# Optimization experiments

Measured on AMD Instinct MI355X. Metric: run time of the kernel, lower is better.

## Reference

```python
import jax, jax.numpy as jnp
import numpy as np

TOPK = 64  # init kwarg: number of dst routes kept per src node


def setup_inputs() -> dict:
    key = jax.random.key(0)
    ks = jax.random.split(key, 6)
    B, J, K, D, Dd = 4, 4096, 8192, 64, 64  # batch, src_nodes, dst_nodes, src_dim, dst_dim
    val = jax.random.normal(ks[0], (B, J, D), jnp.float32)
    state = jax.random.normal(ks[1], (B, J), jnp.float32)
    dst_state = jax.random.normal(ks[2], (B, K), jnp.float32)
    dst_val = jax.random.normal(ks[3], (B, K, Dd), jnp.float32)
    W_route = jax.random.normal(ks[4], (D, K), jnp.float32) / np.sqrt(D).astype(np.float32)
    W_val = jax.random.normal(ks[5], (D, Dd), jnp.float32) / np.sqrt(D).astype(np.float32)
    return dict(val=val, state=state, dst_state=dst_state, dst_val=dst_val,
                W_route=W_route, W_val=W_val)


def _sparse_routes(logits, topk):
    # top-k indices per src node, scatter a bool mask, masked softmax over dst axis
    _, idx = jax.lax.top_k(logits, topk)              # [B, J, topk]
    B, J, K = logits.shape
    mask = jnp.zeros((B, J, K), dtype=bool)
    mask = mask.at[jnp.arange(B)[:, None, None],
                   jnp.arange(J)[None, :, None], idx].set(True)
    neg = jnp.finfo(logits.dtype).min
    return jax.nn.softmax(jnp.where(mask, logits, neg), axis=-1)


def reference(val, state, dst_state, dst_val, W_route, W_val):
    # route_fn: linear over src val -> logits [B, J, K]
    logits = jnp.einsum('bjd,dk->bjk', val, W_route)
    routes = _sparse_routes(logits, TOPK)             # sparse masked softmax
    projected_val = jnp.einsum('bjd,de->bje', val, W_val)  # val_proj_fn (Linear)
    projected_state = state                            # state_proj_fn = Identity
    sender = jax.nn.softplus(state)                    # state_activation_fn
    weighted = routes * sender[..., None]              # [B, J, K]
    delta_state = jnp.einsum('bjk,bj->bk', weighted, projected_state)
    delta_val = jnp.einsum('bjk,bjd->bkd', weighted, projected_val)
    # merge_mode='add'
    return (dst_state + delta_state, dst_val + delta_val)
```

## Files before the change

kernel.cpp:

```cpp
#include <hip/hip_runtime.h>
#include <math.h>

#define NB 4
#define J 4096
#define KDIM 8192
#define DDIM 64
#define DD 64
#define TOPK 64

#define BM 32
#define THREADS 512
#define NITER 16
#define CAP 256
#define BCAP 96
#define OVFCAP (NB * J * TOPK)

typedef _Float16 half8_t __attribute__((ext_vector_type(8)));
typedef float f32x16 __attribute__((ext_vector_type(16)));
union H8 { half8_t h; uint4 u; };
__device__ __forceinline__ half8_t as_h8(uint4 v) { H8 x; x.u = v; return x.h; }

__device__ __forceinline__ unsigned f2key(float f) {
  unsigned u = __float_as_uint(f);
  return u ^ (unsigned)(((int)u >> 31) | 0x80000000);
}
__device__ __forceinline__ float key2f(unsigned k) {
  unsigned u = (k & 0x80000000u) ? (k & 0x7FFFFFFFu) : ~k;
  return __uint_as_float(u);
}
__device__ __forceinline__ unsigned wred_maxu(unsigned v) {
  #pragma unroll
  for (int o = 32; o > 0; o >>= 1) { unsigned u = __shfl_xor(v, o, 64); v = u > v ? u : v; }
  return v;
}
__device__ __forceinline__ unsigned wred_minu(unsigned v) {
  #pragma unroll
  for (int o = 32; o > 0; o >>= 1) { unsigned u = __shfl_xor(v, o, 64); v = u < v ? u : v; }
  return v;
}
__device__ __forceinline__ float wred_addf(float v) {
  #pragma unroll
  for (int o = 32; o > 0; o >>= 1) v += __shfl_xor(v, o, 64);
  return v;
}

__device__ __forceinline__ void route_append(
    unsigned* counts, uint2* bucket, unsigned* ovf_cnt, uint2* ovf,
    int b, unsigned kk, unsigned jloc, float w)
{
  const size_t bk = (size_t)b * KDIM + kk;
  const unsigned slot = atomicAdd(&counts[bk], 1u);
  if (slot < BCAP) {
    bucket[bk * BCAP + slot] = make_uint2(__float_as_uint(w), jloc);
  } else {
    const unsigned op = atomicAdd(ovf_cnt, 1u);
    if (op < (unsigned)OVFCAP)
      ovf[op] = make_uint2(__float_as_uint(w), ((unsigned)bk << 12) | jloc);
  }
}

__global__ void k_prep(const float* __restrict__ W, unsigned* __restrict__ WFh,
                       float* __restrict__ WT)
{
  __shared__ _Float16 lh[64][64];
  __shared__ float lf[64][64];
  const int t = threadIdx.x;
  const int kb = blockIdx.x * 64;
  for (int i = t; i < 4096; i += 256) {
    const int d = i >> 6, c = i & 63;
    const float x = W[(size_t)d * KDIM + kb + c];
    lh[c][d] = (_Float16)x;
    lf[c][d] = x;
  }
  __syncthreads();
  for (int q = t; q < 512; q += 256) {
    const int gt2 = q >> 8, rem = q & 255;
    const int ks = rem >> 6, lane = rem & 63;
    const int c = gt2 * 32 + (lane & 31);
    const int d0 = ks * 16 + (lane >> 5) * 8;
    const int gtile = blockIdx.x * 2 + gt2;
    const size_t off = ((size_t)(gtile * 4 + ks) * 64 + lane) * 4;
    *(uint4*)(WFh + off) = *(const uint4*)&lh[c][d0];
  }
  for (int q = t; q < 1024; q += 256) {
    const int c = q >> 4, d0 = (q & 15) * 4;
    *(float4*)(WT + (size_t)(kb + c) * DDIM + d0) = *(const float4*)&lf[c][d0];
  }
}

__global__ __launch_bounds__(THREADS, 4) void k_routes(
    const float* __restrict__ val, const float* __restrict__ state,
    const unsigned* __restrict__ WFh, const float* __restrict__ WT,
    const float* __restrict__ W_val, float* __restrict__ pv,
    unsigned* __restrict__ counts, uint2* __restrict__ bucket,
    unsigned* __restrict__ flags, unsigned* __restrict__ ovf_cnt,
    uint2* __restrict__ ovf)
{
  __shared__ __align__(16) float val_lds[BM][DDIM + 4];
  __shared__ unsigned short cand_idx[BM][CAP];
  __shared__ unsigned have[BM];
  __shared__ float tauF[BM];

  const int t = threadIdx.x;
  const int lane = t & 63;
  const int wv = t >> 6;
  const int hi = lane >> 5;
  const int lane31 = lane & 31;
  const int row0 = blockIdx.x * BM;
  const int b = row0 / J;

  {
    const int r = t >> 4, d0 = (t & 15) * 4;
    const float4 v4 = *(const float4*)(val + (size_t)(row0 + r) * DDIM + d0);
    val_lds[r][d0] = v4.x; val_lds[r][d0 + 1] = v4.y;
    val_lds[r][d0 + 2] = v4.z; val_lds[r][d0 + 3] = v4.w;
  }
  __syncthreads();

  if (t < BM) {
    float n2 = 0.f;
    #pragma unroll
    for (int d = 0; d < DDIM; ++d) { const float x = val_lds[t][d]; n2 = fmaf(x, x, n2); }
    tauF[t] = 0.26f * sqrtf(n2);
    have[t] = 0u;
  }

  half8_t ah[4];
  {
    const int m = lane31;
    #pragma unroll
    for (int ks = 0; ks < 4; ++ks) {
      const int d0 = ks * 16 + hi * 8;
      #pragma unroll
      for (int j = 0; j < 8; ++j) ah[ks][j] = (_Float16)val_lds[m][d0 + j];
    }
  }
  __syncthreads();

  float taufr[16];
  #pragma unroll
  for (int r = 0; r < 16; ++r) taufr[r] = tauF[(r & 3) + 8 * (r >> 2) + 4 * hi];

  const unsigned* wpBase = WFh + (size_t)(wv * 2) * 1024 + lane * 4;
  const unsigned* wp = wpBase;
  uint4 b0 = *(const uint4*)(wp);        uint4 b1 = *(const uint4*)(wp + 256);
  uint4 b2 = *(const uint4*)(wp + 512);  uint4 b3 = *(const uint4*)(wp + 768);
  uint4 b4 = *(const uint4*)(wp + 1024); uint4 b5 = *(const uint4*)(wp + 1280);
  uint4 b6 = *(const uint4*)(wp + 1536); uint4 b7 = *(const uint4*)(wp + 1792);

  #pragma unroll 1
  for (int it = 0; it < NITER; ++it) {
    f32x16 acc0, acc1;
    #pragma unroll
    for (int i = 0; i < 16; ++i) { acc0[i] = 0.f; acc1[i] = 0.f; }
    acc0 = __builtin_amdgcn_mfma_f32_32x32x16_f16(ah[0], as_h8(b0), acc0, 0, 0, 0);
    acc1 = __builtin_amdgcn_mfma_f32_32x32x16_f16(ah[0], as_h8(b4), acc1, 0, 0, 0);
    acc0 = __builtin_amdgcn_mfma_f32_32x32x16_f16(ah[1], as_h8(b1), acc0, 0, 0, 0);
    acc1 = __builtin_amdgcn_mfma_f32_32x32x16_f16(ah[1], as_h8(b5), acc1, 0, 0, 0);
    acc0 = __builtin_amdgcn_mfma_f32_32x32x16_f16(ah[2], as_h8(b2), acc0, 0, 0, 0);
    acc1 = __builtin_amdgcn_mfma_f32_32x32x16_f16(ah[2], as_h8(b6), acc1, 0, 0, 0);
    acc0 = __builtin_amdgcn_mfma_f32_32x32x16_f16(ah[3], as_h8(b3), acc0, 0, 0, 0);
    acc1 = __builtin_amdgcn_mfma_f32_32x32x16_f16(ah[3], as_h8(b7), acc1, 0, 0, 0);

    const unsigned colbase = (unsigned)((it * 16 + wv * 2) * 32 + lane31);

    wp = (it == NITER - 1) ? wpBase : wp + 16384;
    b0 = *(const uint4*)(wp);        b1 = *(const uint4*)(wp + 256);
    b2 = *(const uint4*)(wp + 512);  b3 = *(const uint4*)(wp + 768);
    b4 = *(const uint4*)(wp + 1024); b5 = *(const uint4*)(wp + 1280);
    b6 = *(const uint4*)(wp + 1536); b7 = *(const uint4*)(wp + 1792);

    #pragma unroll
    for (int r = 0; r < 16; ++r) {
      const int row = (r & 3) + 8 * (r >> 2) + 4 * hi;
      const float tf = taufr[r];
      if (acc0[r] > tf) {
        const unsigned slot = atomicAdd(&have[row], 1u);
        if (slot < CAP) cand_idx[row][slot] = (unsigned short)colbase;
      }
      if (acc1[r] > tf) {
        const unsigned slot = atomicAdd(&have[row], 1u);
        if (slot < CAP) cand_idx[row][slot] = (unsigned short)(colbase + 32);
      }
    }
  }
  __syncthreads();

  {
    const int r = t >> 4, e0 = (t & 15) * 4;
    float a0 = 0.f, a1 = 0.f, a2 = 0.f, a3 = 0.f;
    #pragma unroll 8
    for (int d = 0; d < DDIM; ++d) {
      const float v = val_lds[r][d];
      const float4 w4 = *(const float4*)(W_val + (size_t)d * DD + e0);
      a0 = fmaf(v, w4.x, a0); a1 = fmaf(v, w4.y, a1);
      a2 = fmaf(v, w4.z, a2); a3 = fmaf(v, w4.w, a3);
    }
    *(float4*)(pv + (size_t)(row0 + r) * DD + e0) = make_float4(a0, a1, a2, a3);
  }

  for (int rr = 0; rr < 4; ++rr) {
    const int r = wv * 4 + rr;
    const int row = row0 + r;
    const unsigned hv = have[r];
    if (hv > CAP || hv < TOPK) {
      if (lane == 0) flags[row] = 1u;
      continue;
    }
    const int nc = (int)hv;
    unsigned k4[4]; unsigned id4[4];
    #pragma unroll
    for (int i = 0; i < 4; ++i) {
      const int s = i * 64 + lane;
      k4[i] = 0u; id4[i] = 0xFFFFFFFFu;
      if (s < nc) {
        const unsigned kk = (unsigned)cand_idx[r][s];
        id4[i] = kk;
        const float* wt = WT + (size_t)kk * DDIM;
        float a = 0.f;
        #pragma unroll
        for (int d = 0; d < DDIM; d += 4) {
          const float4 w4 = *(const float4*)(wt + d);
          a = fmaf(val_lds[r][d], w4.x, a);
          a = fmaf(val_lds[r][d + 1], w4.y, a);
          a = fmaf(val_lds[r][d + 2], w4.z, a);
          a = fmaf(val_lds[r][d + 3], w4.w, a);
        }
        k4[i] = f2key(a);
      }
    }
    unsigned lmax = k4[0];
    #pragma unroll
    for (int i = 1; i < 4; ++i) lmax = k4[i] > lmax ? k4[i] : lmax;
    const unsigned kmaxAll = wred_maxu(lmax);
    unsigned klo = f2key(0.99f * tauF[r]); if (klo == 0u) klo = 1u;
    unsigned khi = kmaxAll + 1u;
    auto cge4 = [&](unsigned th) {
      int c = 0;
      #pragma unroll
      for (int i = 0; i < 4; ++i) c += __popcll(__ballot(k4[i] >= th));
      return c;
    };
    int cnt = nc;
    while (cnt != TOPK && khi - klo > 1u) {
      const unsigned mid = klo + ((khi - klo) >> 1);
      const int c = cge4(mid);
      if (c >= TOPK) { klo = mid; cnt = c; } else khi = mid;
    }
    const unsigned thr = klo;
    if (key2f(thr) <= 1.006f * tauF[r]) {
      if (lane == 0) flags[row] = 1u;
      continue;
    }
    unsigned selmask = 0u;
    if (cnt == TOPK) {
      #pragma unroll
      for (int i = 0; i < 4; ++i) if (k4[i] >= thr) selmask |= 1u << i;
    } else {
      #pragma unroll
      for (int i = 0; i < 4; ++i) if (k4[i] > thr) selmask |= 1u << i;
      int tot = 0;
      #pragma unroll
      for (int i = 0; i < 4; ++i) tot += __popcll(__ballot((selmask >> i) & 1));
      int need = TOPK - tot;
      while (need > 0) {
        unsigned best = 0xFFFFFFFFu; int bi = -1;
        #pragma unroll
        for (int i = 0; i < 4; ++i)
          if (k4[i] == thr && !(selmask & (1u << i)) && id4[i] < best) { best = id4[i]; bi = i; }
        const unsigned g = wred_minu(best);
        if (g == 0xFFFFFFFFu) break;
        if (bi >= 0 && best == g) selmask |= 1u << bi;
        --need;
      }
    }
    const float m = key2f(kmaxAll);
    float p[4]; float lsum = 0.f;
    #pragma unroll
    for (int i = 0; i < 4; ++i) {
      p[i] = 0.f;
      if (selmask & (1u << i)) { p[i] = __expf(key2f(k4[i]) - m); lsum += p[i]; }
    }
    lsum = wred_addf(lsum);
    const float st = state[row];
    const float sender = st > 20.f ? st : log1pf(__expf(st));
    const float scale = sender / lsum;
    const unsigned jloc = (unsigned)(row & (J - 1));
    #pragma unroll
    for (int i = 0; i < 4; ++i) {
      if (selmask & (1u << i))
        route_append(counts, bucket, ovf_cnt, ovf, b, id4[i], jloc, p[i] * scale);
    }
  }
}

__global__ void k_fix(const float* __restrict__ val, const float* __restrict__ state,
                      const float* __restrict__ W, const unsigned* __restrict__ flags,
                      unsigned* __restrict__ counts, uint2* __restrict__ bucket,
                      unsigned* __restrict__ ovf_cnt, uint2* __restrict__ ovf)
{
  __shared__ unsigned anyf;
  __shared__ unsigned lsk[64][TOPK + 1];
  __shared__ unsigned short lsi[64][TOPK];
  const int t = threadIdx.x;
  const int row = blockIdx.x * 64 + t;
  if (t == 0) anyf = 0u;
  __syncthreads();
  const unsigned f = flags[row];
  if (f) anyf = 1u;
  __syncthreads();
  if (!anyf) return;
  if (!f) return;

  float v[DDIM];
  #pragma unroll
  for (int d = 0; d < DDIM; ++d) v[d] = val[(size_t)row * DDIM + d];
  int m = 0, worst = 0;
  for (int k = 0; k < KDIM; ++k) {
    float acc = 0.f;
    #pragma unroll 8
    for (int d = 0; d < DDIM; ++d) acc = fmaf(v[d], W[(size_t)d * KDIM + k], acc);
    const unsigned key = f2key(acc);
    if (m < TOPK) {
      lsk[t][m] = key; lsi[t][m] = (unsigned short)k; ++m;
      if (m == TOPK) {
        worst = 0;
        for (int q = 1; q < TOPK; ++q)
          if (lsk[t][q] < lsk[t][worst] ||
              (lsk[t][q] == lsk[t][worst] && lsi[t][q] > lsi[t][worst])) worst = q;
      }
    } else if (key > lsk[t][worst]) {
      lsk[t][worst] = key; lsi[t][worst] = (unsigned short)k;
      worst = 0;
      for (int q = 1; q < TOPK; ++q)
        if (lsk[t][q] < lsk[t][worst] ||
            (lsk[t][q] == lsk[t][worst] && lsi[t][q] > lsi[t][worst])) worst = q;
    }
  }
  unsigned km = lsk[t][0];
  for (int q = 1; q < TOPK; ++q) if (lsk[t][q] > km) km = lsk[t][q];
  const float mx = key2f(km);
  float lsum = 0.f;
  for (int q = 0; q < TOPK; ++q) lsum += __expf(key2f(lsk[t][q]) - mx);
  const float st = state[row];
  const float sender = st > 20.f ? st : log1pf(__expf(st));
  const float scale = sender / lsum;
  const int b = row / J;
  const unsigned jloc = (unsigned)(row & (J - 1));
  for (int q = 0; q < TOPK; ++q) {
    const float w = __expf(key2f(lsk[t][q]) - mx) * scale;
    route_append(counts, bucket, ovf_cnt, ovf, b, (unsigned)lsi[t][q], jloc, w);
  }
}

__global__ void k_gather(const unsigned* __restrict__ counts,
                         const uint2* __restrict__ bucket, const float* __restrict__ pv,
                         const float* __restrict__ state,
                         const float* __restrict__ dst_state,
                         const float* __restrict__ dst_val,
                         float* __restrict__ out_state, float* __restrict__ out_val)
{
  const int wv = threadIdx.x >> 6, lane = threadIdx.x & 63;
  const size_t bk = (size_t)blockIdx.x * 4 + wv;
  unsigned n = counts[bk];
  if (n > BCAP) n = BCAP;
  const int b = (int)(bk >> 13);
  const size_t jbase = (size_t)b * J;
  const uint2* __restrict__ bb = bucket + bk * BCAP;
  float a0 = 0.f, a1 = 0.f, a2 = 0.f, a3 = 0.f;
  float s0 = 0.f, s1 = 0.f, s2 = 0.f, s3 = 0.f;
  unsigned i = 0;
  for (; i + 4 <= n; i += 4) {
    const uint2 e0 = bb[i + 0], e1 = bb[i + 1], e2 = bb[i + 2], e3 = bb[i + 3];
    const float w0 = __uint_as_float(e0.x), w1 = __uint_as_float(e1.x);
    const float w2 = __uint_as_float(e2.x), w3 = __uint_as_float(e3.x);
    a0 = fmaf(w0, pv[(jbase + e0.y) * DD + lane], a0);
    a1 = fmaf(w1, pv[(jbase + e1.y) * DD + lane], a1);
    a2 = fmaf(w2, pv[(jbase + e2.y) * DD + lane], a2);
    a3 = fmaf(w3, pv[(jbase + e3.y) * DD + lane], a3);
    s0 = fmaf(w0, state[jbase + e0.y], s0); s1 = fmaf(w1, state[jbase + e1.y], s1);
    s2 = fmaf(w2, state[jbase + e2.y], s2); s3 = fmaf(w3, state[jbase + e3.y], s3);
  }
  for (; i < n; ++i) {
    const uint2 e = bb[i];
    const float w = __uint_as_float(e.x);
    a0 = fmaf(w, pv[(jbase + e.y) * DD + lane], a0);
    s0 = fmaf(w, state[jbase + e.y], s0);
  }
  const size_t o = bk * DD + lane;
  out_val[o] = dst_val[o] + ((a0 + a1) + (a2 + a3));
  if (lane == 0) out_state[bk] = dst_state[bk] + ((s0 + s1) + (s2 + s3));
}

__global__ void k_ovf(const unsigned* __restrict__ ovf_cnt, const uint2* __restrict__ ovf,
                      const float* __restrict__ pv, const float* __restrict__ state,
                      float* __restrict__ out_state, float* __restrict__ out_val)
{
  unsigned n = *ovf_cnt;
  if (n > (unsigned)OVFCAP) n = (unsigned)OVFCAP;
  const unsigned wglob = (blockIdx.x * blockDim.x + threadIdx.x) >> 6;
  const int lane = threadIdx.x & 63;
  const unsigned nw = (gridDim.x * blockDim.x) >> 6;
  for (unsigned i = wglob; i < n; i += nw) {
    const uint2 e = ovf[i];
    const float w = __uint_as_float(e.x);
    const unsigned bk = e.y >> 12;
    const unsigned j = e.y & (J - 1);
    const size_t jg = (size_t)(bk >> 13) * J + j;
    atomicAdd(&out_val[(size_t)bk * DD + lane], w * pv[jg * DD + lane]);
    if (lane == 0) atomicAdd(&out_state[bk], w * state[jg]);
  }
}

extern "C" void kernel_launch(void* const* d_in, const int* in_sizes, int n_in,
                              void* d_out, int out_size, void* d_ws, size_t ws_size,
                              hipStream_t stream)
{
  (void)in_sizes; (void)n_in; (void)out_size; (void)ws_size;
  const float* val       = (const float*)d_in[0];
  const float* state     = (const float*)d_in[1];
  const float* dst_state = (const float*)d_in[2];
  const float* dst_val   = (const float*)d_in[3];
  const float* W_route   = (const float*)d_in[4];
  const float* W_val     = (const float*)d_in[5];
  float* out_state = (float*)d_out;
  float* out_val   = out_state + (size_t)NB * KDIM;

  char* p = (char*)d_ws;
  unsigned* counts  = (unsigned*)p;  p += (size_t)NB * KDIM * 4;
  unsigned* flags   = (unsigned*)p;  p += (size_t)NB * J * 4;
  unsigned* ovf_cnt = (unsigned*)p;  p += 256;
  float* pv         = (float*)p;     p += (size_t)NB * J * DD * 4;
  unsigned* WFh     = (unsigned*)p;  p += (size_t)KDIM * DDIM * 2;
  float* WT         = (float*)p;     p += (size_t)KDIM * DDIM * 4;
  uint2* bucket     = (uint2*)p;     p += (size_t)NB * KDIM * BCAP * 8;
  uint2* ovf        = (uint2*)p;     p += (size_t)OVFCAP * 8;

  hipMemsetAsync(counts, 0, (size_t)NB * KDIM * 4 + (size_t)NB * J * 4 + 256, stream);

  hipLaunchKernelGGL(k_prep, dim3(KDIM / 64), dim3(256), 0, stream, W_route, WFh, WT);
  hipLaunchKernelGGL(k_routes, dim3(NB * J / BM), dim3(THREADS), 0, stream,
                     val, state, WFh, WT, W_val, pv, counts, bucket, flags, ovf_cnt, ovf);
  hipLaunchKernelGGL(k_fix, dim3(NB * J / 64), dim3(64), 0, stream,
                     val, state, W_route, flags, counts, bucket, ovf_cnt, ovf);
  hipLaunchKernelGGL(k_gather, dim3(NB * KDIM / 4), dim3(256), 0, stream,
                     counts, bucket, pv, state, dst_state, dst_val, out_state, out_val);
  hipLaunchKernelGGL(k_ovf, dim3(256), dim3(256), 0, stream,
                     ovf_cnt, ovf, pv, state, out_state, out_val);
}
```

Measured before the change: 218.8 us.

## Split route kernel into half-K candidate pass and per-row select kernel

The fused routing kernel is split in two. A candidate kernel runs on a 2D grid, each block scanning half of the destination columns with MFMA, and writes thresholded candidate indices to global memory. A separate select kernel then gives each row its own wavefront, rescores the candidates in fp32 with a lane-split dot product, and does the top-k selection and softmax. The aim is more parallelism, higher occupancy and better balance of the serial per-row selection work. The cost is an extra launch, a global round trip for candidates, and a smaller per-half candidate cap, which may push more rows to the fallback path. The overflow buffer is also shrunk.

```diff
diff --git a/kernel.cpp b/kernel.cpp
--- a/kernel.cpp
+++ b/kernel.cpp
@@ -10,10 +10,11 @@
 
 #define BM 32
 #define THREADS 512
-#define NITER 16
-#define CAP 256
+#define NITER_H 8
+#define CAP_H 128
+#define GCAP 256
 #define BCAP 96
-#define OVFCAP (NB * J * TOPK)
+#define OVFCAP 65536
 
 typedef _Float16 half8_t __attribute__((ext_vector_type(8)));
 typedef float f32x16 __attribute__((ext_vector_type(16)));
@@ -88,16 +89,14 @@
   }
 }
 
-__global__ __launch_bounds__(THREADS, 4) void k_routes(
-    const float* __restrict__ val, const float* __restrict__ state,
-    const unsigned* __restrict__ WFh, const float* __restrict__ WT,
+__global__ __launch_bounds__(THREADS, 6) void k_cand(
+    const float* __restrict__ val, const unsigned* __restrict__ WFh,
     const float* __restrict__ W_val, float* __restrict__ pv,
-    unsigned* __restrict__ counts, uint2* __restrict__ bucket,
-    unsigned* __restrict__ flags, unsigned* __restrict__ ovf_cnt,
-    uint2* __restrict__ ovf)
+    unsigned short* __restrict__ gidx, unsigned* __restrict__ gcnt,
+    float* __restrict__ gtau, unsigned* __restrict__ flags)
 {
   __shared__ __align__(16) float val_lds[BM][DDIM + 4];
-  __shared__ unsigned short cand_idx[BM][CAP];
+  __shared__ unsigned short cand_idx[BM][CAP_H];
   __shared__ unsigned have[BM];
   __shared__ float tauF[BM];
 
@@ -107,7 +106,7 @@
   const int hi = lane >> 5;
   const int lane31 = lane & 31;
   const int row0 = blockIdx.x * BM;
-  const int b = row0 / J;
+  const int h = blockIdx.y;
 
   {
     const int r = t >> 4, d0 = (t & 15) * 4;
@@ -123,6 +122,7 @@
     for (int d = 0; d < DDIM; ++d) { const float x = val_lds[t][d]; n2 = fmaf(x, x, n2); }
     tauF[t] = 0.26f * sqrtf(n2);
     have[t] = 0u;
+    if (h == 0) gtau[row0 + t] = tauF[t];
   }
 
   half8_t ah[4];
@@ -141,7 +141,7 @@
   #pragma unroll
   for (int r = 0; r < 16; ++r) taufr[r] = tauF[(r & 3) + 8 * (r >> 2) + 4 * hi];
 
-  const unsigned* wpBase = WFh + (size_t)(wv * 2) * 1024 + lane * 4;
+  const unsigned* wpBase = WFh + (size_t)(h * 128 + wv * 2) * 1024 + lane * 4;
   const unsigned* wp = wpBase;
   uint4 b0 = *(const uint4*)(wp);        uint4 b1 = *(const uint4*)(wp + 256);
   uint4 b2 = *(const uint4*)(wp + 512);  uint4 b3 = *(const uint4*)(wp + 768);
@@ -149,7 +149,7 @@
   uint4 b6 = *(const uint4*)(wp + 1536); uint4 b7 = *(const uint4*)(wp + 1792);
 
   #pragma unroll 1
-  for (int it = 0; it < NITER; ++it) {
+  for (int it = 0; it < NITER_H; ++it) {
     f32x16 acc0, acc1;
     #pragma unroll
     for (int i = 0; i < 16; ++i) { acc0[i] = 0.f; acc1[i] = 0.f; }
@@ -162,9 +162,9 @@
     acc0 = __builtin_amdgcn_mfma_f32_32x32x16_f16(ah[3], as_h8(b3), acc0, 0, 0, 0);
     acc1 = __builtin_amdgcn_mfma_f32_32x32x16_f16(ah[3], as_h8(b7), acc1, 0, 0, 0);
 
-    const unsigned colbase = (unsigned)((it * 16 + wv * 2) * 32 + lane31);
-
-    wp = (it == NITER - 1) ? wpBase : wp + 16384;
+    const unsigned colbase = (unsigned)((h * 128 + it * 16 + wv * 2) * 32 + lane31);
+
+    wp = (it == NITER_H - 1) ? wpBase : wp + 16384;
     b0 = *(const uint4*)(wp);        b1 = *(const uint4*)(wp + 256);
     b2 = *(const uint4*)(wp + 512);  b3 = *(const uint4*)(wp + 768);
     b4 = *(const uint4*)(wp + 1024); b5 = *(const uint4*)(wp + 1280);
@@ -176,17 +176,16 @@
       const float tf = taufr[r];
       if (acc0[r] > tf) {
         const unsigned slot = atomicAdd(&have[row], 1u);
-        if (slot < CAP) cand_idx[row][slot] = (unsigned short)colbase;
+        if (slot < CAP_H) cand_idx[row][slot] = (unsigned short)colbase;
       }
       if (acc1[r] > tf) {
         const unsigned slot = atomicAdd(&have[row], 1u);
-        if (slot < CAP) cand_idx[row][slot] = (unsigned short)(colbase + 32);
+        if (slot < CAP_H) cand_idx[row][slot] = (unsigned short)(colbase + 32);
       }
     }
   }
-  __syncthreads();
-
-  {
+
+  if (h == 1) {
     const int r = t >> 4, e0 = (t & 15) * 4;
     float a0 = 0.f, a1 = 0.f, a2 = 0.f, a3 = 0.f;
     #pragma unroll 8
@@ -199,98 +198,149 @@
     *(float4*)(pv + (size_t)(row0 + r) * DD + e0) = make_float4(a0, a1, a2, a3);
   }
 
-  for (int rr = 0; rr < 4; ++rr) {
-    const int r = wv * 4 + rr;
-    const int row = row0 + r;
+  __syncthreads();
+
+  for (int i = t; i < BM * CAP_H; i += THREADS) {
+    const int r = i >> 7, s = i & (CAP_H - 1);
     const unsigned hv = have[r];
-    if (hv > CAP || hv < TOPK) {
-      if (lane == 0) flags[row] = 1u;
-      continue;
-    }
-    const int nc = (int)hv;
-    unsigned k4[4]; unsigned id4[4];
-    #pragma unroll
-    for (int i = 0; i < 4; ++i) {
-      const int s = i * 64 + lane;
-      k4[i] = 0u; id4[i] = 0xFFFFFFFFu;
-      if (s < nc) {
-        const unsigned kk = (unsigned)cand_idx[r][s];
-        id4[i] = kk;
-        const float* wt = WT + (size_t)kk * DDIM;
-        float a = 0.f;
-        #pragma unroll
-        for (int d = 0; d < DDIM; d += 4) {
-          const float4 w4 = *(const float4*)(wt + d);
-          a = fmaf(val_lds[r][d], w4.x, a);
-          a = fmaf(val_lds[r][d + 1], w4.y, a);
-          a = fmaf(val_lds[r][d + 2], w4.z, a);
-          a = fmaf(val_lds[r][d + 3], w4.w, a);
-        }
-        k4[i] = f2key(a);
+    const int lim = hv < CAP_H ? (int)hv : CAP_H;
+    if (s < lim)
+      gidx[(size_t)(row0 + r) * GCAP + h * CAP_H + s] = cand_idx[r][s];
+  }
+  if (t < BM) {
+    const unsigned hv = have[t];
+    gcnt[(size_t)(row0 + t) * 2 + h] = hv < CAP_H ? hv : CAP_H;
+    if (hv > CAP_H) flags[row0 + t] = 1u;
+  }
+}
+
+__global__ __launch_bounds__(THREADS, 6) void k_select(
+    const float* __restrict__ val, const float* __restrict__ state,
+    const float* __restrict__ WT,
+    const unsigned short* __restrict__ gidx, const unsigned* __restrict__ gcnt,
+    const float* __restrict__ gtau, unsigned* __restrict__ flags,
+    unsigned* __restrict__ counts, uint2* __restrict__ bucket,
+    unsigned* __restrict__ ovf_cnt, uint2* __restrict__ ovf)
+{
+  __shared__ float skey[THREADS / 64][GCAP];
+  const int t = threadIdx.x;
+  const int lane = t & 63;
+  const int wv = t >> 6;
+  const int row = blockIdx.x * (THREADS / 64) + wv;
+
+  if (flags[row]) return;
+  const int c0 = (int)gcnt[(size_t)row * 2];
+  const int c1 = (int)gcnt[(size_t)row * 2 + 1];
+  const int nc = c0 + c1;
+  if (nc < TOPK) { if (lane == 0) flags[row] = 1u; return; }
+  const float tau = gtau[row];
+
+  const int cq = lane >> 2;
+  const int dq = lane & 3;
+  float4 v4[4];
+  #pragma unroll
+  for (int j = 0; j < 4; ++j)
+    v4[j] = *(const float4*)(val + (size_t)row * DDIM + dq * 16 + j * 4);
+
+  unsigned id4[4];
+  #pragma unroll
+  for (int i = 0; i < 4; ++i) {
+    const int s = i * 64 + lane;
+    id4[i] = 0xFFFFFFFFu;
+    if (s < nc) {
+      const int ps = s < c0 ? s : (s - c0 + CAP_H);
+      id4[i] = (unsigned)gidx[(size_t)row * GCAP + ps];
+    }
+  }
+
+  for (int s0 = 0; s0 < nc; s0 += 16) {
+    const int s = s0 + cq;
+    float a = 0.f;
+    if (s < nc) {
+      const int ps = s < c0 ? s : (s - c0 + CAP_H);
+      const unsigned kk = (unsigned)gidx[(size_t)row * GCAP + ps];
+      const float* wt = WT + (size_t)kk * DDIM + dq * 16;
+      #pragma unroll
+      for (int j = 0; j < 4; ++j) {
+        const float4 w4 = *(const float4*)(wt + j * 4);
+        a = fmaf(v4[j].x, w4.x, a); a = fmaf(v4[j].y, w4.y, a);
+        a = fmaf(v4[j].z, w4.z, a); a = fmaf(v4[j].w, w4.w, a);
       }
     }
-    unsigned lmax = k4[0];
-    #pragma unroll
-    for (int i = 1; i < 4; ++i) lmax = k4[i] > lmax ? k4[i] : lmax;
-    const unsigned kmaxAll = wred_maxu(lmax);
-    unsigned klo = f2key(0.99f * tauF[r]); if (klo == 0u) klo = 1u;
-    unsigned khi = kmaxAll + 1u;
-    auto cge4 = [&](unsigned th) {
-      int c = 0;
+    a += __shfl_xor(a, 1, 64); a += __shfl_xor(a, 2, 64);
+    if (dq == 0 && s < nc) skey[wv][s] = a;
+  }
+  asm volatile("s_waitcnt lgkmcnt(0)" ::: "memory");
+  __builtin_amdgcn_sched_barrier(0);
+
+  unsigned k4[4];
+  #pragma unroll
+  for (int i = 0; i < 4; ++i) {
+    const int s = i * 64 + lane;
+    k4[i] = (s < nc) ? f2key(skey[wv][s]) : 0u;
+  }
+  unsigned lmax = k4[0];
+  #pragma unroll
+  for (int i = 1; i < 4; ++i) lmax = k4[i] > lmax ? k4[i] : lmax;
+  const unsigned kmaxAll = wred_maxu(lmax);
+  unsigned klo = f2key(0.99f * tau); if (klo == 0u) klo = 1u;
+  unsigned khi = kmaxAll + 1u;
+  auto cge4 = [&](unsigned th) {
+    int c = 0;
+    #pragma unroll
+    for (int i = 0; i < 4; ++i) c += __popcll(__ballot(k4[i] >= th));
+    return c;
+  };
+  int cnt = nc;
+  while (cnt != TOPK && khi - klo > 1u) {
+    const unsigned mid = klo + ((khi - klo) >> 1);
+    const int c = cge4(mid);
+    if (c >= TOPK) { klo = mid; cnt = c; } else khi = mid;
+  }
+  const unsigned thr = klo;
+  if (key2f(thr) <= 1.006f * tau) {
+    if (lane == 0) flags[row] = 1u;
+    return;
+  }
+  unsigned selmask = 0u;
+  if (cnt == TOPK) {
+    #pragma unroll
+    for (int i = 0; i < 4; ++i) if (k4[i] >= thr) selmask |= 1u << i;
+  } else {
+    #pragma unroll
+    for (int i = 0; i < 4; ++i) if (k4[i] > thr) selmask |= 1u << i;
+    int tot = 0;
+    #pragma unroll
+    for (int i = 0; i < 4; ++i) tot += __popcll(__ballot((selmask >> i) & 1));
+    int need = TOPK - tot;
+    while (need > 0) {
+      unsigned best = 0xFFFFFFFFu; int bi = -1;
       #pragma unroll
-      for (int i = 0; i < 4; ++i) c += __popcll(__ballot(k4[i] >= th));
-      return c;
-    };
-    int cnt = nc;
-    while (cnt != TOPK && khi - klo > 1u) {
-      const unsigned mid = klo + ((khi - klo) >> 1);
-      const int c = cge4(mid);
-      if (c >= TOPK) { klo = mid; cnt = c; } else khi = mid;
-    }
-    const unsigned thr = klo;
-    if (key2f(thr) <= 1.006f * tauF[r]) {
-      if (lane == 0) flags[row] = 1u;
-      continue;
-    }
-    unsigned selmask = 0u;
-    if (cnt == TOPK) {
-      #pragma unroll
-      for (int i = 0; i < 4; ++i) if (k4[i] >= thr) selmask |= 1u << i;
-    } else {
-      #pragma unroll
-      for (int i = 0; i < 4; ++i) if (k4[i] > thr) selmask |= 1u << i;
-      int tot = 0;
-      #pragma unroll
-      for (int i = 0; i < 4; ++i) tot += __popcll(__ballot((selmask >> i) & 1));
-      int need = TOPK - tot;
-      while (need > 0) {
-        unsigned best = 0xFFFFFFFFu; int bi = -1;
-        #pragma unroll
-        for (int i = 0; i < 4; ++i)
-          if (k4[i] == thr && !(selmask & (1u << i)) && id4[i] < best) { best = id4[i]; bi = i; }
-        const unsigned g = wred_minu(best);
-        if (g == 0xFFFFFFFFu) break;
-        if (bi >= 0 && best == g) selmask |= 1u << bi;
-        --need;
-      }
-    }
-    const float m = key2f(kmaxAll);
-    float p[4]; float lsum = 0.f;
-    #pragma unroll
-    for (int i = 0; i < 4; ++i) {
-      p[i] = 0.f;
-      if (selmask & (1u << i)) { p[i] = __expf(key2f(k4[i]) - m); lsum += p[i]; }
-    }
-    lsum = wred_addf(lsum);
-    const float st = state[row];
-    const float sender = st > 20.f ? st : log1pf(__expf(st));
-    const float scale = sender / lsum;
-    const unsigned jloc = (unsigned)(row & (J - 1));
-    #pragma unroll
-    for (int i = 0; i < 4; ++i) {
-      if (selmask & (1u << i))
-        route_append(counts, bucket, ovf_cnt, ovf, b, id4[i], jloc, p[i] * scale);
-    }
+      for (int i = 0; i < 4; ++i)
+        if (k4[i] == thr && !(selmask & (1u << i)) && id4[i] < best) { best = id4[i]; bi = i; }
+      const unsigned g = wred_minu(best);
+      if (g == 0xFFFFFFFFu) break;
+      if (bi >= 0 && best == g) selmask |= 1u << bi;
+      --need;
+    }
+  }
+  const float m = key2f(kmaxAll);
+  float p[4]; float lsum = 0.f;
+  #pragma unroll
+  for (int i = 0; i < 4; ++i) {
+    p[i] = 0.f;
+    if (selmask & (1u << i)) { p[i] = __expf(key2f(k4[i]) - m); lsum += p[i]; }
+  }
+  lsum = wred_addf(lsum);
+  const float st = state[row];
+  const float sender = st > 20.f ? st : log1pf(__expf(st));
+  const float scale = sender / lsum;
+  const int b = row / J;
+  const unsigned jloc = (unsigned)(row & (J - 1));
+  #pragma unroll
+  for (int i = 0; i < 4; ++i) {
+    if (selmask & (1u << i))
+      route_append(counts, bucket, ovf_cnt, ovf, b, id4[i], jloc, p[i] * scale);
   }
 }
 
@@ -430,17 +480,25 @@
   unsigned* counts  = (unsigned*)p;  p += (size_t)NB * KDIM * 4;
   unsigned* flags   = (unsigned*)p;  p += (size_t)NB * J * 4;
   unsigned* ovf_cnt = (unsigned*)p;  p += 256;
+  unsigned* gcnt    = (unsigned*)p;  p += (size_t)NB * J * 2 * 4;
   float* pv         = (float*)p;     p += (size_t)NB * J * DD * 4;
   unsigned* WFh     = (unsigned*)p;  p += (size_t)KDIM * DDIM * 2;
   float* WT         = (float*)p;     p += (size_t)KDIM * DDIM * 4;
+  float* gtau       = (float*)p;     p += (size_t)NB * J * 4;
+  unsigned short* gidx = (unsigned short*)p; p += (size_t)NB * J * GCAP * 2;
   uint2* bucket     = (uint2*)p;     p += (size_t)NB * KDIM * BCAP * 8;
   uint2* ovf        = (uint2*)p;     p += (size_t)OVFCAP * 8;
 
-  hipMemsetAsync(counts, 0, (size_t)NB * KDIM * 4 + (size_t)NB * J * 4 + 256, stream);
+  hipMemsetAsync(counts, 0,
+                 (size_t)NB * KDIM * 4 + (size_t)NB * J * 4 + 256 +
+                 (size_t)NB * J * 2 * 4, stream);
 
   hipLaunchKernelGGL(k_prep, dim3(KDIM / 64), dim3(256), 0, stream, W_route, WFh, WT);
-  hipLaunchKernelGGL(k_routes, dim3(NB * J / BM), dim3(THREADS), 0, stream,
-                     val, state, WFh, WT, W_val, pv, counts, bucket, flags, ovf_cnt, ovf);
+  hipLaunchKernelGGL(k_cand, dim3(NB * J / BM, 2), dim3(THREADS), 0, stream,
+                     val, WFh, W_val, pv, gidx, gcnt, gtau, flags);
+  hipLaunchKernelGGL(k_select, dim3(NB * J / (THREADS / 64)), dim3(THREADS), 0, stream,
+                     val, state, WT, gidx, gcnt, gtau, flags,
+                     counts, bucket, ovf_cnt, ovf);
   hipLaunchKernelGGL(k_fix, dim3(NB * J / 64), dim3(64), 0, stream,
                      val, state, W_route, flags, counts, bucket, ovf_cnt, ovf);
   hipLaunchKernelGGL(k_gather, dim3(NB * KDIM / 4), dim3(256), 0, stream,
```

After: 323.6 us. 47.9% more time.
